# Kernel optimization log

Measured on AMD Instinct MI355X. Metric: run time of the kernel, lower is better.

Reference implementation:

```python
import jax, jax.numpy as jnp
import numpy as np

NEG_INF = -1e30  # safe -inf surrogate to avoid nan in logsumexp


def _ctc_loss_sum(log_probs, labels, input_lengths, label_lengths):
    # log_probs: (T, N, C) already log-softmaxed; blank = 0
    T, N, C = log_probs.shape
    S = labels.shape[1]
    L = 2 * S + 1  # extended label sequence: blank-interleaved

    # extended labels: [blank, y1, blank, y2, ..., blank]
    ext = jnp.zeros((N, L), dtype=jnp.int32).at[:, 1::2].set(labels.astype(jnp.int32))
    # gather emission log-probs for extended labels: (T, N, L)
    lp_ext = jnp.take_along_axis(log_probs, jnp.broadcast_to(ext[None], (T, N, L)), axis=2)

    # transition from l-2 allowed only for non-blank labels differing from ext[l-2]
    ext_m2 = jnp.pad(ext, ((0, 0), (2, 0)), constant_values=-1)[:, :L]
    allow_skip = (ext != 0) & (ext != ext_m2)  # (N, L)

    # alpha at t=0
    alpha0 = jnp.full((N, L), NEG_INF, dtype=log_probs.dtype)
    alpha0 = alpha0.at[:, 0].set(lp_ext[0, :, 0])
    alpha0 = alpha0.at[:, 1].set(jnp.where(label_lengths > 0, lp_ext[0, :, 1], NEG_INF))

    def step(alpha, t_and_lp):
        t, lp_t = t_and_lp  # lp_t: (N, L)
        a1 = jnp.pad(alpha, ((0, 0), (1, 0)), constant_values=NEG_INF)[:, :L]
        a2 = jnp.pad(alpha, ((0, 0), (2, 0)), constant_values=NEG_INF)[:, :L]
        a2 = jnp.where(allow_skip, a2, NEG_INF)
        m = jnp.maximum(jnp.maximum(alpha, a1), a2)
        lse = m + jnp.log(jnp.exp(alpha - m) + jnp.exp(a1 - m) + jnp.exp(a2 - m))
        new = jnp.where(m > NEG_INF / 2, lse + lp_t, NEG_INF)
        # freeze alpha past each sequence's input length
        alpha = jnp.where((t < input_lengths)[:, None], new, alpha)
        return alpha, None

    alpha, _ = jax.lax.scan(step, alpha0, (jnp.arange(1, T), lp_ext[1:]))

    # log-likelihood = logsumexp(alpha[2*Sl], alpha[2*Sl - 1])
    idx = (2 * label_lengths).astype(jnp.int32)
    a_last = jnp.take_along_axis(alpha, idx[:, None], axis=1)[:, 0]
    a_prev = jnp.take_along_axis(alpha, jnp.maximum(idx - 1, 0)[:, None], axis=1)[:, 0]
    a_prev = jnp.where(label_lengths > 0, a_prev, NEG_INF)
    m = jnp.maximum(a_last, a_prev)
    ll = m + jnp.log(jnp.exp(a_last - m) + jnp.exp(a_prev - m))
    loss = -ll
    # zero_infinity=True: replace infinite losses with 0
    loss = jnp.where(loss < -NEG_INF / 2, loss, 0.0)
    return jnp.sum(loss)


def setup_inputs() -> dict:
    T, N, C, S = 512, 32, 4000, 64
    key = jax.random.key(0)
    k1, k2 = jax.random.split(key)
    inputs = jax.random.normal(k1, (T, N, C), dtype=jnp.float32)
    labels = jax.random.randint(k2, (N, S), 1, C, dtype=jnp.int32)  # exclude blank=0
    input_lengths = jnp.full((N,), T, dtype=jnp.int32)
    label_lengths = jnp.full((N,), S, dtype=jnp.int32)
    return {"inputs": inputs, "labels": labels,
            "input_lengths": input_lengths, "label_lengths": label_lengths}


def reference(inputs, labels, input_lengths, label_lengths):
    log_probs = jax.nn.log_softmax(inputs, axis=2)
    return _ctc_loss_sum(log_probs, labels, input_lengths, label_lengths)
```

## Files before the change

### kernel.cpp

```cpp
#include <hip/hip_runtime.h>

#define LN2 0.6931471805599453f

constexpr int T = 512, N = 32, C = 4000, S = 64;
constexpr int TN   = T * N;
constexpr int ROWF = 68;
constexpr int CT   = 16;
constexpr int CTB  = 8;
constexpr int QROWS = 4096;

__device__ __forceinline__ float dpp_shr1_zero(float x) {
    int r = __builtin_amdgcn_update_dpp(0, __float_as_int(x),
                                        0x138 , 0xf, 0xf, false);
    return __int_as_float(r);
}
__device__ __forceinline__ float dpp_shl1_zero(float x) {
    int r = __builtin_amdgcn_update_dpp(0, __float_as_int(x),
                                        0x130 , 0xf, 0xf, false);
    return __int_as_float(r);
}
template <int CTRL>
__device__ __forceinline__ float dpp_max_step(float x) {
    int t = __builtin_amdgcn_update_dpp(__float_as_int(x), __float_as_int(x),
                                        CTRL, 0xf, 0xf, false);
    return fmaxf(x, __int_as_float(t));
}
__device__ __forceinline__ float wave_max_bcast(float x) {
    x = dpp_max_step<0xB1>(x);  x = dpp_max_step<0x4E>(x);
    x = dpp_max_step<0x141>(x); x = dpp_max_step<0x140>(x);
    x = dpp_max_step<0x142>(x); x = dpp_max_step<0x143>(x);
    return __int_as_float(__builtin_amdgcn_readlane(__float_as_int(x), 63));
}

__device__ __forceinline__ void softmax_row(
    const float* __restrict__ x, const int* __restrict__ labels,
    float* __restrict__ pp, float* __restrict__ ee, int row, int lane)
{
    const float*  rp  = x + (size_t)row * C;
    const float4* rp4 = reinterpret_cast<const float4*>(rp);

    float m = -INFINITY, s = 0.f;
    #pragma unroll
    for (int k = 0; k < 15; ++k) {
        float4 v = rp4[lane + 64 * k];
        float mv = fmaxf(fmaxf(v.x, v.y), fmaxf(v.z, v.w));
        float s4 = __expf(v.x - mv) + __expf(v.y - mv) +
                   __expf(v.z - mv) + __expf(v.w - mv);
        float nm = fmaxf(m, mv);
        s = s * __expf(m - nm) + s4 * __expf(mv - nm);
        m = nm;
    }
    if (lane < 40) {
        float4 v = rp4[960 + lane];
        float mv = fmaxf(fmaxf(v.x, v.y), fmaxf(v.z, v.w));
        float s4 = __expf(v.x - mv) + __expf(v.y - mv) +
                   __expf(v.z - mv) + __expf(v.w - mv);
        float nm = fmaxf(m, mv);
        s = s * __expf(m - nm) + s4 * __expf(mv - nm);
        m = nm;
    }
    for (int off = 32; off; off >>= 1) {
        float om = __shfl_xor(m, off), os = __shfl_xor(s, off);
        float nm = fmaxf(m, om);
        s = s * __expf(m - nm) + os * __expf(om - nm);
        m = nm;
    }
    float logZ = m + __logf(s);

    int t = row >> 5, n = row & 31;
    int c  = labels[n * S + lane];
    float zb = rp[0];
    float zl = rp[c];

    float wm = zl;
    for (int off = 32; off; off >>= 1) wm = fmaxf(wm, __shfl_xor(wm, off));
    wm = fmaxf(wm, zb);
    float pm = __expf(wm - logZ);
    int e = (int)(__float_as_uint(pm) >> 23) - 127;

    float* outp = pp + ((size_t)n * T + t) * ROWF;
    outp[1 + lane] = ldexpf(__expf(zl - logZ), -e);
    if (lane == 0) {
        outp[0] = ldexpf(__expf(zb - logZ), -e);
        ee[n * T + t] = (float)e;
    }
}

__global__ __launch_bounds__(256) void k_phase(
    const float* __restrict__ x, const int* __restrict__ labels,
    float* __restrict__ pp, float* __restrict__ ee, float* __restrict__ gst,
    const int* __restrict__ in_len, const int* __restrict__ lab_len,
    int qrow0, int ttop, int first)
{
    __shared__ __align__(16) float ldsB[4][2][CTB][ROWF];
    const int wid = threadIdx.x >> 6, lane = threadIdx.x & 63;

    if (blockIdx.x >= 8) {
        softmax_row(x, labels, pp, ee,
                    qrow0 + ((int)blockIdx.x - 8) * 4 + wid, lane);
        return;
    }
    if (ttop < 0) return;
    const int n = blockIdx.x * 4 + wid;
    const int Tin = in_len[n], Sl = lab_len[n];
    if (Tin != T) return;
    const float* bp = pp + (size_t)n * T * ROWF;

    const int li = labels[n * S + lane];
    const int lim1 = lane ? labels[n * S + lane - 1] : -1;
    const float skf = (lane > 0 && li != 0 && li != lim1) ? 1.f : 0.f;
    const float skD = dpp_shl1_zero(skf);

    float* st = gst + n * 136;
    float g0, g1, gX;
    int SHb;
    if (first) {
        g0 = (lane == Sl) ? 1.f : 0.f;
        g1 = (Sl > 0 && lane == Sl - 1) ? 1.f : 0.f;
        gX = (Sl >= S && lane == 63) ? 1.f : 0.f;
        SHb = 0;
    } else {
        float2 g = *reinterpret_cast<const float2*>(&st[2 * lane]);
        g0 = g.x; g1 = g.y;
        gX = (lane == 63) ? st[128] : 0.f;
        SHb = (int)st[129];
    }
    asm volatile("s_waitcnt vmcnt(0)" ::: "memory");
    __builtin_amdgcn_sched_barrier(0);

#define ISSUEB(cc) do {                                                       \
    const float* cp_ = bp + (size_t)(ttop - 7 - 8 * (cc)) * ROWF;             \
    if (lane < 17) {                                                          \
        _Pragma("unroll")                                                     \
        for (int d_ = 0; d_ < CTB; ++d_)                                      \
            __builtin_amdgcn_global_load_lds(cp_ + (size_t)d_ * ROWF + lane * 4, \
                                             &ldsB[wid][(cc) & 1][d_][0], 16, 0, 0); \
    } } while (0)

#define BSTEPP(B, D) do {                                                     \
    const float* R_ = &ldsB[wid][B][D][0];                                    \
    float cb_ = R_[0], cl_ = R_[1 + lane];                                    \
    float cD_ = dpp_shl1_zero(cl_);                         \
    float d1_ = dpp_shl1_zero(g1);                           \
    float d0s_ = dpp_shl1_zero(g0);                          \
    float d0_ = (lane == 63) ? gX : d0s_;                                     \
    float cg_ = cl_ * g1;                                                     \
    float ng0 = fmaf(cb_, g0, cg_);                                           \
    float ng1 = fmaf(skD * cD_, d1_, fmaf(cb_, d0_, cg_));                    \
    float ngX = cb_ * gX;                                                     \
    g0 = ng0; g1 = ng1; gX = ngX;                                             \
} while (0)

#define BRENORM do {                                                          \
    float g_ = wave_max_bcast(fmaxf(g0, fmaxf(g1, gX)));                      \
    unsigned b_ = __float_as_uint(g_);                                        \
    int k_ = (b_ == 0u) ? 0 : (100 - ((int)(b_ >> 23) - 127));                \
    g0 = ldexpf(g0, k_); g1 = ldexpf(g1, k_); gX = ldexpf(gX, k_);            \
    SHb += k_;                                                                \
} while (0)

    ISSUEB(0); ISSUEB(1);
    for (int c = 0; c < 16; ++c) {
        if (c < 15) { asm volatile("s_waitcnt vmcnt(8)" ::: "memory"); }
        else        { asm volatile("s_waitcnt vmcnt(0)" ::: "memory"); }
        __builtin_amdgcn_sched_barrier(0);
        int buf = c & 1;
        BSTEPP(buf, 7); BSTEPP(buf, 6); BSTEPP(buf, 5); BSTEPP(buf, 4);
        BRENORM;
        BSTEPP(buf, 3); BSTEPP(buf, 2); BSTEPP(buf, 1); BSTEPP(buf, 0);
        BRENORM;
        if (c + 2 < 16) {
            __builtin_amdgcn_sched_barrier(0);
            ISSUEB(c + 2);
        }
    }

    float2 gv; gv.x = g0; gv.y = g1;
    *reinterpret_cast<float2*>(&st[2 * lane]) = gv;
    if (lane == 63) { st[128] = gX; st[129] = (float)SHb; }
#undef BRENORM
#undef BSTEPP
#undef ISSUEB
}

__global__ __launch_bounds__(128) void k_final(
    const float* __restrict__ pp, const float* __restrict__ ee,
    float* __restrict__ gst, const int* __restrict__ labels,
    const int* __restrict__ in_len, const int* __restrict__ lab_len,
    float* __restrict__ loss_out)
{
    __shared__ __align__(16) float ldsF[2][CT][ROWF];
    __shared__ __align__(16) float ldsT[2][CT][ROWF];
    __shared__ float gj[132];
    const int n = blockIdx.x;
    const int wid = threadIdx.x >> 6, lane = threadIdx.x & 63;
    const int Tin = in_len[n], Sl = lab_len[n];
    const float* bp = pp + (size_t)n * T * ROWF;
    const bool hot = (Tin == T);

    const int li   = labels[n * S + lane];
    const int lim1 = lane ? labels[n * S + lane - 1] : -1;
    const float skf  = (lane > 0 && li != 0 && li != lim1) ? 1.f : 0.f;
    const float skUf = dpp_shr1_zero(skf);
    const float skk  = skf * skUf;
    const float skD  = dpp_shl1_zero(skf);

    float a0 = 0.f, a1 = 0.f, aX = 0.f;
    int SH = 0;

#define ISSUE_F(cc) do {                                                      \
    const float* cp_ = bp + (size_t)(cc) * CT * ROWF;                         \
    if (lane < 17) {                                                          \
        _Pragma("unroll")                                                     \
        for (int d_ = 0; d_ < CT; ++d_)                                       \
            __builtin_amdgcn_global_load_lds(cp_ + (size_t)d_ * ROWF + lane * 4, \
                                             &ldsF[(cc) & 1][d_][0], 16, 0, 0); \
    } } while (0)
#define ISSUE_T(cc) do {                                                      \
    const float* cp_ = bp + (size_t)(112 - 16 * (cc)) * ROWF;                 \
    if (lane < 17) {                                                          \
        _Pragma("unroll")                                                     \
        for (int d_ = 0; d_ < CT; ++d_)                                       \
            __builtin_amdgcn_global_load_lds(cp_ + (size_t)d_ * ROWF + lane * 4, \
                                             &ldsT[(cc) & 1][d_][0], 16, 0, 0); \
    } } while (0)

#define PAIRS(B, D) do {                                                      \
    const float* R0_ = &ldsF[B][D][0];                                        \
    const float* R1_ = &ldsF[B][(D) + 1][0];                                  \
    float cb1 = R0_[0], cl1 = R0_[1 + lane];                                  \
    float cb2 = R1_[0], cl2 = R1_[1 + lane];                                  \
    float clU = dpp_shr1_zero(cl1);                                           \
    float W   = clU * cl2;                                                    \
    float A   = cb1 * cb2;                                                    \
    float B_  = clU * cb2;                                                    \
    float Cc  = A + B_;                                                       \
    float D_  = skUf * B_;                                                    \
    float s1  = cb1 + cl1;                                                    \
    float E   = s1 * cl2;                                                     \
    float F   = cl1 * cl2;                                                    \
    float G   = skf * W;                                                      \
    float H   = fmaf(skf, F + W, cb1 * cl2);                                  \
    float I   = skk * W;                                                      \
    float Y0  = cl1 * cb2;                                                    \
    float Y1  = s1 * cb2;                                                     \
    float Y2  = skf * Y0;                                                     \
    float p1  = dpp_shr1_zero(a1);                                            \
    float p0  = dpp_shr1_zero(a0);                                            \
    float p2  = dpp_shr1_zero(p1);                                            \
    float n0  = fmaf(p0, B_, a0 * A) + fmaf(p2, D_, p1 * Cc);                 \
    float n1  = fmaf(a1, F, a0 * E) + fmaf(p2, I, fmaf(p1, H, p0 * G));       \
    float nX  = fmaf(a1, Y1, aX * A) + fmaf(p1, Y2, a0 * Y0);                 \
    a0 = n0; a1 = n1; aX = nX;                                                \
} while (0)

#define WINDOW4(B, D0) do {                                                   \
    a0 = ldexpf(a0, kA); a1 = ldexpf(a1, kA); aX = ldexpf(aX, kA);            \
    SH += kA;                                                                 \
    float gnow_ = fmaxf(fmaxf(a0, a1), aX);                                   \
    PAIRS(B, D0);                                                             \
    gs = dpp_max_step<0xB1>(gs);  gs = dpp_max_step<0x4E>(gs);                \
    PAIRS(B, (D0) + 2);                                                       \
    gs = dpp_max_step<0x141>(gs); gs = dpp_max_step<0x140>(gs);               \
    PAIRS(B, (D0) + 4);                                                       \
    gs = dpp_max_step<0x142>(gs); gs = dpp_max_step<0x143>(gs);               \
    PAIRS(B, (D0) + 6);                                                       \
    {   unsigned b_ = (unsigned)__builtin_amdgcn_readlane(__float_as_int(gs), 63); \
        int e_ = (int)(b_ >> 23) - 127;                                       \
        kA = (b_ == 0u) ? 0 : (105 - e_ - kA);                                \
    }                                                                         \
    gs = gnow_;                                                               \
} while (0)

#define BSTEPT(B, D) do {                                                     \
    const float* R_ = &ldsT[B][D][0];                                         \
    float cb_ = R_[0], cl_ = R_[1 + lane];                                    \
    float cD_ = dpp_shl1_zero(cl_);                                           \
    float d1_ = dpp_shl1_zero(g1);                                            \
    float d0s_ = dpp_shl1_zero(g0);                                           \
    float d0_ = (lane == 63) ? gX : d0s_;                                     \
    float cg_ = cl_ * g1;                                                     \
    float ng0 = fmaf(cb_, g0, cg_);                                           \
    float ng1 = fmaf(skD * cD_, d1_, fmaf(cb_, d0_, cg_));                    \
    float ngX = cb_ * gX;                                                     \
    g0 = ng0; g1 = ng1; gX = ngX;                                             \
} while (0)
#define BRENORM do {                                                          \
    float g_ = wave_max_bcast(fmaxf(g0, fmaxf(g1, gX)));                      \
    unsigned b_ = __float_as_uint(g_);                                        \
    int k_ = (b_ == 0u) ? 0 : (100 - ((int)(b_ >> 23) - 127));                \
    g0 = ldexpf(g0, k_); g1 = ldexpf(g1, k_); gX = ldexpf(gX, k_);            \
    SHb += k_;                                                                \
} while (0)

    asm volatile("s_waitcnt vmcnt(0)" ::: "memory");
    __builtin_amdgcn_sched_barrier(0);

    if (wid == 0) {
        if (hot) {
            int kA = 0; float gs = 0.f;
            ISSUE_F(0); ISSUE_F(1);
            asm volatile("s_waitcnt vmcnt(16)" ::: "memory");
            __builtin_amdgcn_sched_barrier(0);
            a0 = (lane == 0) ? ldsF[0][0][0] : 0.f;
            a1 = (lane == 0 && Sl > 0) ? ldsF[0][0][1] : 0.f;
            {
                float cb = ldsF[0][1][0], cl = ldsF[0][1][1 + lane];
                float p1 = dpp_shr1_zero(a1);
                float n0 = (a0 + p1) * cb;
                float n1 = fmaf(skf, p1, a0 + a1) * cl;
                float nX = (aX + a1) * cb;
                a0 = n0; a1 = n1; aX = nX;
            }
            PAIRS(0, 2); PAIRS(0, 4); PAIRS(0, 6);
            {   float g = wave_max_bcast(fmaxf(fmaxf(a0, a1), aX));
                unsigned b = __float_as_uint(g);
                int k0 = (b == 0u) ? 0 : (105 - ((int)(b >> 23) - 127));
                a0 = ldexpf(a0, k0); a1 = ldexpf(a1, k0); aX = ldexpf(aX, k0);
                SH += k0; kA = 0;
                gs = fmaxf(fmaxf(a0, a1), aX);
            }
            WINDOW4(0, 8);
            __builtin_amdgcn_sched_barrier(0);
            ISSUE_F(2);
            for (int c = 1; c < 4; ++c) {
                if (c < 3) { asm volatile("s_waitcnt vmcnt(16)" ::: "memory"); }
                else       { asm volatile("s_waitcnt vmcnt(0)"  ::: "memory"); }
                __builtin_amdgcn_sched_barrier(0);
                int buf = c & 1;
                WINDOW4(buf, 0);
                WINDOW4(buf, 8);
                if (c + 2 < 4) {
                    __builtin_amdgcn_sched_barrier(0);
                    ISSUE_F(c + 2);
                }
            }
        } else {
#define GSTEP(cc, dd) do {                                                    \
    float cb_ = ldsF[(cc) & 1][dd][0];                                        \
    float cl_ = ldsF[(cc) & 1][dd][1 + lane];                                 \
    float p1_ = dpp_shr1_zero(a1);                                            \
    float na0_ = (a0 + p1_) * cb_;                                            \
    float na1_ = fmaf(skf, p1_, a0 + a1) * cl_;                               \
    float naX_ = (aX + a1) * cb_;                                             \
    int t_ = (cc) * CT + (dd);                                                \
    bool act_ = (unsigned)(t_ - 1) < (unsigned)(Tin - 1);                     \
    a0 = act_ ? na0_ : a0;                                                    \
    a1 = act_ ? na1_ : a1;                                                    \
    aX = act_ ? naX_ : aX;                                                    \
    if (((dd) & 3) == 3) {                                                    \
        float g_ = wave_max_bcast(fmaxf(a0, fmaxf(a1, aX)));                  \
        unsigned b_ = __float_as_uint(g_);                                    \
        int k_ = (b_ == 0u) ? 0 : (100 - ((int)(b_ >> 23) - 127));            \
        a0 = ldexpf(a0, k_); a1 = ldexpf(a1, k_); aX = ldexpf(aX, k_);        \
        SH += k_;                                                             \
    }                                                                         \
} while (0)
            ISSUE_F(0); ISSUE_F(1);
            asm volatile("s_waitcnt vmcnt(16)" ::: "memory");
            __builtin_amdgcn_sched_barrier(0);
            a0 = (lane == 0) ? ldsF[0][0][0] : 0.f;
            a1 = (lane == 0 && Sl > 0) ? ldsF[0][0][1] : 0.f;
            #pragma unroll
            for (int d = 1; d < CT; ++d) GSTEP(0, d);
            __builtin_amdgcn_sched_barrier(0);
            ISSUE_F(2);
            for (int c = 1; c < T / CT; ++c) {
                if (c < T / CT - 1) { asm volatile("s_waitcnt vmcnt(16)" ::: "memory"); }
                else                { asm volatile("s_waitcnt vmcnt(0)"  ::: "memory"); }
                __builtin_amdgcn_sched_barrier(0);
                #pragma unroll
                for (int d = 0; d < CT; ++d) GSTEP(c, d);
                if (c + 2 < T / CT) {
                    __builtin_amdgcn_sched_barrier(0);
                    ISSUE_F(c + 2);
                }
            }
#undef GSTEP
        }
    } else if (hot) {
        float* st = gst + n * 136;
        float2 g = *reinterpret_cast<const float2*>(&st[2 * lane]);
        float g0 = g.x, g1 = g.y;
        float gX = (lane == 63) ? st[128] : 0.f;
        int SHb = (int)st[129];

        ISSUE_T(0); ISSUE_T(1);
        for (int c = 0; c < 4; ++c) {
            if (c < 3) { asm volatile("s_waitcnt vmcnt(16)" ::: "memory"); }
            else       { asm volatile("s_waitcnt vmcnt(0)"  ::: "memory"); }
            __builtin_amdgcn_sched_barrier(0);
            int buf = c & 1;
            BSTEPT(buf, 15); BSTEPT(buf, 14); BSTEPT(buf, 13); BSTEPT(buf, 12);
            BRENORM;
            BSTEPT(buf, 11); BSTEPT(buf, 10); BSTEPT(buf, 9);  BSTEPT(buf, 8);
            BRENORM;
            BSTEPT(buf, 7);  BSTEPT(buf, 6);  BSTEPT(buf, 5);  BSTEPT(buf, 4);
            BRENORM;
            BSTEPT(buf, 3);  BSTEPT(buf, 2);  BSTEPT(buf, 1);  BSTEPT(buf, 0);
            BRENORM;
            if (c + 2 < 4) {
                __builtin_amdgcn_sched_barrier(0);
                ISSUE_T(c + 2);
            }
        }
        gj[2 * lane]     = ldexpf(g0, -120);
        gj[2 * lane + 1] = ldexpf(g1, -120);
        if (lane == 63) {
            gj[128] = ldexpf(gX, -120);
            gj[130] = (float)SHb;
        }
    }

    __syncthreads();
    if (wid != 0) return;

    float se = 0.f;
    #pragma unroll
    for (int j = 0; j < 8; ++j) {
        int idx = lane + 64 * j;
        float ev = ee[n * T + idx];
        se += (idx < Tin) ? ev : 0.f;
    }
    for (int off = 32; off; off >>= 1) se += __shfl_xor(se, off);

    if (hot) {
        float term = a0 * gj[2 * lane] + a1 * gj[2 * lane + 1];
        if (lane == 63) term = fmaf(aX, gj[128], term);
        for (int off = 32; off; off >>= 1) term += __shfl_xor(term, off);
        if (lane == 0) {
            float SHb = gj[130];
            float ll2  = log2f(term) - (float)SH - SHb + 120.f + se;
            float loss = -ll2 * LN2;
            if (!(loss < 5e29f)) loss = 0.f;
            loss_out[n] = loss;
        }
    } else {
        float a_last = (Sl >= S) ? __shfl(aX, 63) : __shfl(a0, Sl);
        float a_prev_raw = __shfl(a1, (Sl > 0) ? (Sl - 1) : 0);
        float a_prev = (Sl > 0) ? a_prev_raw : 0.f;
        if (lane == 0) {
            float sum  = a_last + a_prev;
            float ll2  = log2f(sum) - (float)SH + se;
            float loss = -ll2 * LN2;
            if (!(loss < 5e29f)) loss = 0.f;
            loss_out[n] = loss;
        }
    }
#undef BRENORM
#undef BSTEPT
#undef WINDOW4
#undef PAIRS
#undef ISSUE_F
#undef ISSUE_T
}

__global__ __launch_bounds__(64) void k_reduce(
    const float* __restrict__ loss, float* __restrict__ out)
{
    int lane = threadIdx.x;
    float v = (lane < N) ? loss[lane] : 0.f;
    for (int off = 32; off; off >>= 1) v += __shfl_xor(v, off);
    if (lane == 0) out[0] = v;
}

extern "C" void kernel_launch(void* const* d_in, const int* in_sizes, int n_in,
                              void* d_out, int out_size, void* d_ws, size_t ws_size,
                              hipStream_t stream) {
    const float* x       = (const float*)d_in[0];
    const int*   labels  = (const int*)d_in[1];
    const int*   in_len  = (const int*)d_in[2];
    const int*   lab_len = (const int*)d_in[3];
    float* out  = (float*)d_out;
    float* pp   = (float*)d_ws;
    float* ee   = pp + (size_t)TN * ROWF + 256;
    float* loss = ee + TN;
    float* gst  = loss + N + 32;

    const int NB = 8 + QROWS / 4;
    k_phase<<<NB, 256, 0, stream>>>(x, labels, pp, ee, gst, in_len, lab_len,
                                    3 * QROWS, -1, 0);
    k_phase<<<NB, 256, 0, stream>>>(x, labels, pp, ee, gst, in_len, lab_len,
                                    2 * QROWS, 511, 1);
    k_phase<<<NB, 256, 0, stream>>>(x, labels, pp, ee, gst, in_len, lab_len,
                                    1 * QROWS, 383, 0);
    k_phase<<<NB, 256, 0, stream>>>(x, labels, pp, ee, gst, in_len, lab_len,
                                    0 * QROWS, 255, 0);
    k_final<<<N, 128, 0, stream>>>(pp, ee, gst, labels, in_len, lab_len, loss);
    k_reduce<<<1, 64, 0, stream>>>(loss, out);
}
```

Baseline: 81.38 us.

## Split pipeline into two halves and fold final reduction into atomic add

The pipeline goes from four quarter-sized phases to two halves. Softmax covers 8192 rows per launch, the backward pass runs 256 timesteps per phase, and the final kernel's forward and backward loops double in length. The separate reduce kernel is removed: the final kernel atomically adds each per-sequence loss into an output zeroed by a memset. This cuts launch count and inter-kernel gaps, but gives less overlap granularity between softmax and the recurrence, and atomic float summation order becomes nondeterministic.

```diff
diff --git a/kernel.cpp b/kernel.cpp
--- a/kernel.cpp
+++ b/kernel.cpp
@@ -7,7 +7,7 @@
 constexpr int ROWF = 68;
 constexpr int CT   = 16;
 constexpr int CTB  = 8;
-constexpr int QROWS = 4096;
+constexpr int HROWS = 8192;
 
 __device__ __forceinline__ float dpp_shr1_zero(float x) {
     int r = __builtin_amdgcn_update_dpp(0, __float_as_int(x),
@@ -90,14 +90,14 @@
     const float* __restrict__ x, const int* __restrict__ labels,
     float* __restrict__ pp, float* __restrict__ ee, float* __restrict__ gst,
     const int* __restrict__ in_len, const int* __restrict__ lab_len,
-    int qrow0, int ttop, int first)
+    int hrow0, int ttop, int first)
 {
     __shared__ __align__(16) float ldsB[4][2][CTB][ROWF];
     const int wid = threadIdx.x >> 6, lane = threadIdx.x & 63;
 
     if (blockIdx.x >= 8) {
         softmax_row(x, labels, pp, ee,
-                    qrow0 + ((int)blockIdx.x - 8) * 4 + wid, lane);
+                    hrow0 + ((int)blockIdx.x - 8) * 4 + wid, lane);
         return;
     }
     if (ttop < 0) return;
@@ -107,8 +107,8 @@
     const float* bp = pp + (size_t)n * T * ROWF;
 
     const int li = labels[n * S + lane];
-    const int lim1 = lane ? labels[n * S + lane - 1] : -1;
-    const float skf = (lane > 0 && li != 0 && li != lim1) ? 1.f : 0.f;
+    const float skf = (lane > 0 && li != 0 &&
+                       li != labels[n * S + lane - 1]) ? 1.f : 0.f;
     const float skD = dpp_shl1_zero(skf);
 
     float* st = gst + n * 136;
@@ -160,8 +160,8 @@
 } while (0)
 
     ISSUEB(0); ISSUEB(1);
-    for (int c = 0; c < 16; ++c) {
-        if (c < 15) { asm volatile("s_waitcnt vmcnt(8)" ::: "memory"); }
+    for (int c = 0; c < 32; ++c) {
+        if (c < 31) { asm volatile("s_waitcnt vmcnt(8)" ::: "memory"); }
         else        { asm volatile("s_waitcnt vmcnt(0)" ::: "memory"); }
         __builtin_amdgcn_sched_barrier(0);
         int buf = c & 1;
@@ -169,7 +169,7 @@
         BRENORM;
         BSTEPP(buf, 3); BSTEPP(buf, 2); BSTEPP(buf, 1); BSTEPP(buf, 0);
         BRENORM;
-        if (c + 2 < 16) {
+        if (c + 2 < 32) {
             __builtin_amdgcn_sched_barrier(0);
             ISSUEB(c + 2);
         }
@@ -187,7 +187,7 @@
     const float* __restrict__ pp, const float* __restrict__ ee,
     float* __restrict__ gst, const int* __restrict__ labels,
     const int* __restrict__ in_len, const int* __restrict__ lab_len,
-    float* __restrict__ loss_out)
+    float* __restrict__ out)
 {
     __shared__ __align__(16) float ldsF[2][CT][ROWF];
     __shared__ __align__(16) float ldsT[2][CT][ROWF];
@@ -217,7 +217,7 @@
                                              &ldsF[(cc) & 1][d_][0], 16, 0, 0); \
     } } while (0)
 #define ISSUE_T(cc) do {                                                      \
-    const float* cp_ = bp + (size_t)(112 - 16 * (cc)) * ROWF;                 \
+    const float* cp_ = bp + (size_t)(240 - 16 * (cc)) * ROWF;                 \
     if (lane < 17) {                                                          \
         _Pragma("unroll")                                                     \
         for (int d_ = 0; d_ < CT; ++d_)                                       \
@@ -323,14 +323,14 @@
             WINDOW4(0, 8);
             __builtin_amdgcn_sched_barrier(0);
             ISSUE_F(2);
-            for (int c = 1; c < 4; ++c) {
-                if (c < 3) { asm volatile("s_waitcnt vmcnt(16)" ::: "memory"); }
+            for (int c = 1; c < 8; ++c) {
+                if (c < 7) { asm volatile("s_waitcnt vmcnt(16)" ::: "memory"); }
                 else       { asm volatile("s_waitcnt vmcnt(0)"  ::: "memory"); }
                 __builtin_amdgcn_sched_barrier(0);
                 int buf = c & 1;
                 WINDOW4(buf, 0);
                 WINDOW4(buf, 8);
-                if (c + 2 < 4) {
+                if (c + 2 < 8) {
                     __builtin_amdgcn_sched_barrier(0);
                     ISSUE_F(c + 2);
                 }
@@ -386,8 +386,8 @@
         int SHb = (int)st[129];
 
         ISSUE_T(0); ISSUE_T(1);
-        for (int c = 0; c < 4; ++c) {
-            if (c < 3) { asm volatile("s_waitcnt vmcnt(16)" ::: "memory"); }
+        for (int c = 0; c < 8; ++c) {
+            if (c < 7) { asm volatile("s_waitcnt vmcnt(16)" ::: "memory"); }
             else       { asm volatile("s_waitcnt vmcnt(0)"  ::: "memory"); }
             __builtin_amdgcn_sched_barrier(0);
             int buf = c & 1;
@@ -399,7 +399,7 @@
             BRENORM;
             BSTEPT(buf, 3);  BSTEPT(buf, 2);  BSTEPT(buf, 1);  BSTEPT(buf, 0);
             BRENORM;
-            if (c + 2 < 4) {
+            if (c + 2 < 8) {
                 __builtin_amdgcn_sched_barrier(0);
                 ISSUE_T(c + 2);
             }
@@ -433,7 +433,7 @@
             float ll2  = log2f(term) - (float)SH - SHb + 120.f + se;
             float loss = -ll2 * LN2;
             if (!(loss < 5e29f)) loss = 0.f;
-            loss_out[n] = loss;
+            atomicAdd(out, loss);
         }
     } else {
         float a_last = (Sl >= S) ? __shfl(aX, 63) : __shfl(a0, Sl);
@@ -444,7 +444,7 @@
             float ll2  = log2f(sum) - (float)SH + se;
             float loss = -ll2 * LN2;
             if (!(loss < 5e29f)) loss = 0.f;
-            loss_out[n] = loss;
+            atomicAdd(out, loss);
         }
     }
 #undef BRENORM
@@ -453,15 +453,6 @@
 #undef PAIRS
 #undef ISSUE_F
 #undef ISSUE_T
-}
-
-__global__ __launch_bounds__(64) void k_reduce(
-    const float* __restrict__ loss, float* __restrict__ out)
-{
-    int lane = threadIdx.x;
-    float v = (lane < N) ? loss[lane] : 0.f;
-    for (int off = 32; off; off >>= 1) v += __shfl_xor(v, off);
-    if (lane == 0) out[0] = v;
 }
 
 extern "C" void kernel_launch(void* const* d_in, const int* in_sizes, int n_in,
@@ -474,18 +465,13 @@
     float* out  = (float*)d_out;
     float* pp   = (float*)d_ws;
     float* ee   = pp + (size_t)TN * ROWF + 256;
-    float* loss = ee + TN;
-    float* gst  = loss + N + 32;
-
-    const int NB = 8 + QROWS / 4;
+    float* gst  = ee + TN + 32;
+
+    hipMemsetAsync(out, 0, sizeof(float), stream);
+    const int NB = 8 + HROWS / 4;
     k_phase<<<NB, 256, 0, stream>>>(x, labels, pp, ee, gst, in_len, lab_len,
-                                    3 * QROWS, -1, 0);
+                                    HROWS, -1, 0);
     k_phase<<<NB, 256, 0, stream>>>(x, labels, pp, ee, gst, in_len, lab_len,
-                                    2 * QROWS, 511, 1);
-    k_phase<<<NB, 256, 0, stream>>>(x, labels, pp, ee, gst, in_len, lab_len,
-                                    1 * QROWS, 383, 0);
-    k_phase<<<NB, 256, 0, stream>>>(x, labels, pp, ee, gst, in_len, lab_len,
-                                    0 * QROWS, 255, 0);
-    k_final<<<N, 128, 0, stream>>>(pp, ee, gst, labels, in_len, lab_len, loss);
-    k_reduce<<<1, 64, 0, stream>>>(loss, out);
-}
+                                    0, 511, 1);
+    k_final<<<N, 128, 0, stream>>>(pp, ee, gst, labels, in_len, lab_len, out);
+}
```

New measurement: 82.13 us. Within noise of the previous version (+0.9%).
